# Optimization experiments

Hardware: AMD Instinct MI355X
Metric: run time of the kernel (lower is better)

## Reference

```python
import jax, jax.numpy as jnp
import numpy as np

B, N, C, R, E = 8, 4096, 128, 16, 65536


def setup_inputs() -> dict:
    key = jax.random.key(0)
    ks = jax.random.split(key, 8)
    node_features = jax.random.normal(ks[0], (B, N, C), dtype=jnp.float32)
    edge_index = jax.random.randint(ks[1], (B, 2, E), 0, N, dtype=jnp.int64)
    edge_type = jax.random.randint(ks[2], (B, E), 0, R, dtype=jnp.int64)
    s = 1.0 / np.sqrt(C)
    rel_weight = jax.random.uniform(ks[3], (R, C, C), jnp.float32, -s, s)
    root_weight = jax.random.uniform(ks[4], (C, C), jnp.float32, -s, s)
    rgcn_bias = jnp.zeros((C,), jnp.float32)
    lin_weight = jax.random.uniform(ks[5], (C, 1), jnp.float32, -s, s)
    lin_bias = jnp.zeros((1,), jnp.float32)
    return {
        'node_features': node_features,
        'edge_index': edge_index,
        'edge_type': edge_type,
        'rel_weight': rel_weight,
        'root_weight': root_weight,
        'rgcn_bias': rgcn_bias,
        'lin_weight': lin_weight,
        'lin_bias': lin_bias,
    }


def _rgcn_score(node_features, edge_index, edge_type, rel_weight, root_weight,
                rgcn_bias, lin_weight, lin_bias):
    # Flatten batch of graphs into one big disjoint graph (as batch_rgcn does).
    x = node_features.reshape(B * N, C)
    offs = (jnp.arange(B, dtype=edge_index.dtype) * N)[:, None, None]  # (B,1,1)
    ei = (edge_index + offs).transpose(1, 0, 2).reshape(2, B * E)  # (2, B*E)
    et = edge_type.reshape(B * E)
    src, dst = ei[0], ei[1]

    x_src = x[src]  # (B*E, C) gathered source features
    # root transform + bias (RGCNConv root_weight + bias)
    out = x @ root_weight + rgcn_bias  # (B*N, C)
    # per-relation mean aggregation; mean(W_r x_j) == W_r mean(x_j)
    for r in range(R):
        mask = (et == r).astype(x.dtype)  # (B*E,)
        s = jax.ops.segment_sum(x_src * mask[:, None], dst, num_segments=B * N)
        cnt = jax.ops.segment_sum(mask, dst, num_segments=B * N)
        mean = jnp.where(cnt[:, None] > 0, s / jnp.maximum(cnt, 1.0)[:, None], 0.0)
        out = out + mean @ rel_weight[r]

    out = jax.nn.relu(out)  # dropout is identity at eval
    scores = (out @ lin_weight + lin_bias).reshape(B, N)
    return scores


def reference(node_features, edge_index, edge_type, rel_weight, root_weight,
              rgcn_bias, lin_weight, lin_bias):
    return _rgcn_score(node_features, edge_index, edge_type, rel_weight,
                       root_weight, rgcn_bias, lin_weight, lin_bias)
```

## Files before the change

### kernel.cpp

```cpp
#include <hip/hip_runtime.h>

#define BB 8
#define NN 4096
#define CC 128
#define RR 16
#define EE 65536
#define NNODES 32768
#define NEDGES 524288
#define BCAP  48
#define SCE   15
#define NT    32
#define ALP   136

typedef unsigned short ushort_t;
typedef short bf16x8 __attribute__((ext_vector_type(8)));
typedef float f32x4 __attribute__((ext_vector_type(4)));

__device__ __forceinline__ unsigned short f2b(float f) {
    unsigned u = __builtin_bit_cast(unsigned, f);
    unsigned r = (u + 0x7fffu + ((u >> 16) & 1u)) >> 16;
    return (unsigned short)r;
}
__device__ __forceinline__ float b2f(unsigned short s) {
    return __builtin_bit_cast(float, (unsigned)s << 16);
}
__device__ __forceinline__ float ldf(const void* p, int j, int isbf) {
    return isbf ? b2f(((const ushort_t*)p)[j]) : ((const float*)p)[j];
}
__device__ __forceinline__ int ldi(const int* p, int j, int is64) {
    return p[j << is64];
}
__device__ __forceinline__ unsigned cvtpk(float lo, float hi) {
    unsigned r;
    asm("v_cvt_pk_bf16_f32 %0, %1, %2" : "=v"(r) : "v"(lo), "v"(hi));
    return r;
}

#define GSUM8(u, sb) do { \
    s[sb+0] += __builtin_bit_cast(float, (u).x << 16); \
    s[sb+1] += __builtin_bit_cast(float, (u).x & 0xffff0000u); \
    s[sb+2] += __builtin_bit_cast(float, (u).y << 16); \
    s[sb+3] += __builtin_bit_cast(float, (u).y & 0xffff0000u); \
    s[sb+4] += __builtin_bit_cast(float, (u).z << 16); \
    s[sb+5] += __builtin_bit_cast(float, (u).z & 0xffff0000u); \
    s[sb+6] += __builtin_bit_cast(float, (u).w << 16); \
    s[sb+7] += __builtin_bit_cast(float, (u).w & 0xffff0000u); \
} while (0)

__global__ __launch_bounds__(256) void prep_k(const void* __restrict__ x,
                                              const void* __restrict__ relw,
                                              const void* __restrict__ rootw,
                                              const int* __restrict__ ei,
                                              const int* __restrict__ et,
                                              ushort_t* __restrict__ Xb,
                                              ushort_t* __restrict__ WT3,
                                              int* __restrict__ dcnt,
                                              int* __restrict__ bucket,
                                              int isbf, int w64i, int w64t) {
    int bx = blockIdx.x, t = threadIdx.x;
    if (bx < 512) {
        int b = bx & 7;
        #pragma unroll
        for (int i = 0; i < 4; ++i) {
            int e = (bx >> 3) * 1024 + i * 256 + t;
            int src = ldi(ei, (b * 2) * EE + e, w64i);
            int dst = ldi(ei, (b * 2 + 1) * EE + e, w64i);
            int r = ldi(et, (b << 16) + e, w64t);
            int gd = (b << 12) + dst;
            int pos = atomicAdd(&dcnt[gd << 4], 1);
            if (pos < BCAP)
                bucket[gd * BCAP + pos] = (((b << 12) + src) << 4) | r;
        }
    } else if (bx < 1024) {
        int bx2 = bx - 512;
        int base = (bx2 & 7) * 65536 + (bx2 >> 3) * 256 + t;
        #pragma unroll
        for (int i = 0; i < 4; ++i) {
            int tid = base + i * 16384;
            if (isbf) {
                ((uint4*)Xb)[tid] = ((const uint4*)x)[tid];
            } else {
                const float4* xf = (const float4*)x;
                float4 a = xf[2 * tid], b = xf[2 * tid + 1];
                ushort4 o0, o1;
                o0.x = f2b(a.x); o0.y = f2b(a.y); o0.z = f2b(a.z); o0.w = f2b(a.w);
                o1.x = f2b(b.x); o1.y = f2b(b.y); o1.z = f2b(b.z); o1.w = f2b(b.w);
                ((ushort4*)Xb)[2 * tid] = o0; ((ushort4*)Xb)[2 * tid + 1] = o1;
            }
        }
    } else {
        __shared__ ushort_t Ls[128 * 40];
        int mb = bx - 1024;
        int mat = mb >> 2, chunk = mb & 3;
        const void* src = (mat == 16) ? rootw : relw;
        int soff = (mat == 16) ? 0 : mat * 16384;
        int k0 = chunk * 32;
        #pragma unroll
        for (int i = 0; i < 16; ++i) {
            int idx = t + i * 256;
            int k = idx >> 7, c = idx & 127;
            Ls[c * 40 + k] = f2b(ldf(src, soff + (k0 + k) * 128 + c, isbf));
        }
        __syncthreads();
        #pragma unroll
        for (int i = 0; i < 2; ++i) {
            int idx = t + i * 256;
            int cg = idx >> 6, lane = idx & 63;
            int lrow = lane & 15, lq = lane >> 4;
            uint4 v = *(const uint4*)(&Ls[(cg * 16 + lrow) * 40 + lq * 8]);
            *(uint4*)(WT3 + ((size_t)((mat * 4 + chunk) * 8 + cg)) * 512 + lane * 8) = v;
        }
    }
}

__global__ __launch_bounds__(512, 4) void agg_k(const ushort_t* __restrict__ Xb,
                                                const ushort_t* __restrict__ WT3,
                                                const int* __restrict__ dcnt,
                                                const int* __restrict__ bucket,
                                                const void* __restrict__ bias,
                                                const void* __restrict__ linw,
                                                const void* __restrict__ linb,
                                                void* __restrict__ out,
                                                int isbf) {
    __shared__ int scnt[NT * 16];
    __shared__ ushort_t srt[NT * 16 * 16];
    __shared__ ushort_t A[2][NT * ALP];
    __shared__ float red[NT][5];
    int bx = blockIdx.x, t = threadIdx.x;
    int n0 = (bx & 7) * NN + (bx >> 3) * NT;

    scnt[t & 511] = 0;
    __syncthreads();

    {
        int ns16 = t >> 4, ts16 = t & 15;
        int gn16 = n0 + ns16;
        int nc = dcnt[gn16 << 4]; if (nc > BCAP) nc = BCAP;
        const int* bk = bucket + gn16 * BCAP;
        for (int j = ts16; j < nc; j += 16) {
            int v = bk[j];
            int row = (ns16 << 4) + (v & 15);
            int pos = atomicAdd(&scnt[row], 1);
            if (pos < SCE)
                srt[(row << 4) + 1 + pos] = (ushort_t)((unsigned)v >> 4);
        }
    }
    __syncthreads();
    srt[t << 4] = (ushort_t)scnt[t];
    __syncthreads();

    int wave = t >> 6, lane = t & 63, lrow = lane & 15, lq = lane >> 4;
    int tg = t & 255;
    int nsub = tg >> 3, tsub = tg & 7;
    int gn = n0 + nsub;
    int offA = tsub * 8, offB = 64 + tsub * 8;
    f32x4 acc[2][2] = {};

    if (wave >= 4) {
        int row = nsub << 4;
        uint4 q0 = *(const uint4*)(&srt[row << 4]);
        int cf = q0.x & 0xffffu; int ce = cf > SCE ? SCE : cf;
        float s[16];
        #pragma unroll
        for (int j = 0; j < 16; ++j) s[j] = 0.f;
        for (int e = 0; e < ce; ++e) {
            int gs = srt[(row << 4) + 1 + e];
            const ushort_t* xr = Xb + (size_t)gs * 128;
            uint4 ua = *(const uint4*)(xr + offA), ub = *(const uint4*)(xr + offB);
            GSUM8(ua, 0); GSUM8(ub, 8);
        }
        float w = (cf > 0) ? 1.0f / (float)cf : 0.f;
        uint4 va, vb;
        va.x = cvtpk(s[0] * w, s[1] * w);   va.y = cvtpk(s[2] * w, s[3] * w);
        va.z = cvtpk(s[4] * w, s[5] * w);   va.w = cvtpk(s[6] * w, s[7] * w);
        vb.x = cvtpk(s[8] * w, s[9] * w);   vb.y = cvtpk(s[10] * w, s[11] * w);
        vb.z = cvtpk(s[12] * w, s[13] * w); vb.w = cvtpk(s[14] * w, s[15] * w);
        *(uint4*)(&A[0][nsub * ALP + offA]) = va;
        *(uint4*)(&A[0][nsub * ALP + offB]) = vb;
    }
    __syncthreads();

    for (int p = 0; p < 17; ++p) {
        int np = p + 1;
        if (wave < 4) {
            const ushort_t* Ap = A[p & 1];
            const ushort_t* bw = WT3 + (size_t)p * 16384 + (wave * 2) * 512 + lane * 8;
            __builtin_amdgcn_s_setprio(1);
            #pragma unroll
            for (int ks = 0; ks < 4; ++ks) {
                int k0 = ks * 32 + lq * 8;
                bf16x8 a0 = *(const bf16x8*)(&Ap[lrow * ALP + k0]);
                bf16x8 a1 = *(const bf16x8*)(&Ap[(16 + lrow) * ALP + k0]);
                bf16x8 b0 = *(const bf16x8*)(bw + ks * 4096);
                bf16x8 b1 = *(const bf16x8*)(bw + ks * 4096 + 512);
                acc[0][0] = __builtin_amdgcn_mfma_f32_16x16x32_bf16(a0, b0, acc[0][0], 0, 0, 0);
                acc[0][1] = __builtin_amdgcn_mfma_f32_16x16x32_bf16(a0, b1, acc[0][1], 0, 0, 0);
                acc[1][0] = __builtin_amdgcn_mfma_f32_16x16x32_bf16(a1, b0, acc[1][0], 0, 0, 0);
                acc[1][1] = __builtin_amdgcn_mfma_f32_16x16x32_bf16(a1, b1, acc[1][1], 0, 0, 0);
            }
            __builtin_amdgcn_s_setprio(0);
        } else if (np < 16) {
            int row = (nsub << 4) + np;
            uint4 q0 = *(const uint4*)(&srt[row << 4]);
            int cf = q0.x & 0xffffu; int ce = cf > SCE ? SCE : cf;
            int e0 = q0.x >> 16, e1 = q0.y & 0xffffu, e2 = q0.y >> 16, e3 = q0.z & 0xffffu;
            uint4 r0a, r0b, r1a, r1b, r2a, r2b, r3a, r3b;
            if (ce > 0) { const ushort_t* xr = Xb + (size_t)e0 * 128; r0a = *(const uint4*)(xr + offA); r0b = *(const uint4*)(xr + offB); }
            if (ce > 1) { const ushort_t* xr = Xb + (size_t)e1 * 128; r1a = *(const uint4*)(xr + offA); r1b = *(const uint4*)(xr + offB); }
            if (ce > 2) { const ushort_t* xr = Xb + (size_t)e2 * 128; r2a = *(const uint4*)(xr + offA); r2b = *(const uint4*)(xr + offB); }
            if (ce > 3) { const ushort_t* xr = Xb + (size_t)e3 * 128; r3a = *(const uint4*)(xr + offA); r3b = *(const uint4*)(xr + offB); }
            float s[16];
            #pragma unroll
            for (int j = 0; j < 16; ++j) s[j] = 0.f;
            if (ce > 0) { GSUM8(r0a, 0); GSUM8(r0b, 8); }
            if (ce > 1) { GSUM8(r1a, 0); GSUM8(r1b, 8); }
            if (ce > 2) { GSUM8(r2a, 0); GSUM8(r2b, 8); }
            if (ce > 3) { GSUM8(r3a, 0); GSUM8(r3b, 8); }
            if (ce > 4) {
                for (int e4 = 4; e4 < ce; ++e4) {
                    int gs = srt[(row << 4) + 1 + e4];
                    const ushort_t* xr = Xb + (size_t)gs * 128;
                    uint4 ta = *(const uint4*)(xr + offA), tb = *(const uint4*)(xr + offB);
                    GSUM8(ta, 0); GSUM8(tb, 8);
                }
            }
            float w = (cf > 0) ? 1.0f / (float)cf : 0.f;
            uint4 va, vb;
            va.x = cvtpk(s[0] * w, s[1] * w);   va.y = cvtpk(s[2] * w, s[3] * w);
            va.z = cvtpk(s[4] * w, s[5] * w);   va.w = cvtpk(s[6] * w, s[7] * w);
            vb.x = cvtpk(s[8] * w, s[9] * w);   vb.y = cvtpk(s[10] * w, s[11] * w);
            vb.z = cvtpk(s[12] * w, s[13] * w); vb.w = cvtpk(s[14] * w, s[15] * w);
            *(uint4*)(&A[np & 1][nsub * ALP + offA]) = va;
            *(uint4*)(&A[np & 1][nsub * ALP + offB]) = vb;
        } else if (np == 16) {
            const ushort_t* xr = Xb + (size_t)gn * 128;
            uint4 r0a = *(const uint4*)(xr + offA), r0b = *(const uint4*)(xr + offB);
            *(uint4*)(&A[np & 1][nsub * ALP + offA]) = r0a;
            *(uint4*)(&A[np & 1][nsub * ALP + offB]) = r0b;
        }
        if (p < 16) __syncthreads();
    }

    if (wave < 4) {
        int wn = wave << 5;
        int c0 = wn + lrow, c1 = wn + 16 + lrow;
        float bi0 = ldf(bias, c0, isbf), bi1 = ldf(bias, c1, isbf);
        float lw0 = ldf(linw, c0, isbf), lw1 = ldf(linw, c1, isbf);
        #pragma unroll
        for (int mi = 0; mi < 2; ++mi)
            #pragma unroll
            for (int rg = 0; rg < 4; ++rg) {
                float p = fmaxf(acc[mi][0][rg] + bi0, 0.f) * lw0
                        + fmaxf(acc[mi][1][rg] + bi1, 0.f) * lw1;
                p += __shfl_xor(p, 1, 64);
                p += __shfl_xor(p, 2, 64);
                p += __shfl_xor(p, 4, 64);
                p += __shfl_xor(p, 8, 64);
                if (lrow == 0) red[mi * 16 + lq * 4 + rg][wave] = p;
            }
    }
    __syncthreads();
    if (t < NT) {
        float res = red[t][0] + red[t][1] + red[t][2] + red[t][3] + ldf(linb, 0, isbf);
        if (isbf) ((ushort_t*)out)[n0 + t] = f2b(res);
        else      ((float*)out)[n0 + t] = res;
    }
}

extern "C" void kernel_launch(void* const* d_in, const int* in_sizes, int n_in,
                              void* d_out, int out_size, void* d_ws, size_t ws_size,
                              hipStream_t stream) {
    const void* x     = d_in[0];
    const int*  ei    = (const int*)d_in[1];
    const int*  et    = (const int*)d_in[2];
    const void* relw  = d_in[3];
    const void* rootw = d_in[4];
    const void* bias  = d_in[5];
    const void* linw  = d_in[6];
    const void* linb  = d_in[7];

    int isbf = (in_sizes[0] == BB * NN * CC * 2);
    int w64i = (in_sizes[1] == BB * 2 * EE * 8);
    int w64t = (in_sizes[2] == BB * EE * 8);

    const size_t WS_NEED = 17334272;
    if (ws_size < WS_NEED) return;

    char* ws = (char*)d_ws;
    ushort_t* Xb     = (ushort_t*)(ws);
    ushort_t* WT3    = (ushort_t*)(ws + 8388608);
    int*      dcnt   = (int*)(ws + 8945664);
    int*      bucket = (int*)(ws + 11042816);

    hipMemsetAsync(dcnt, 0, 2097152, stream);
    prep_k<<<1092, 256, 0, stream>>>(x, relw, rootw, ei, et, Xb, WT3, dcnt, bucket,
                                     isbf, w64i, w64t);
    agg_k<<<1024, 512, 0, stream>>>(Xb, WT3, dcnt, bucket, bias, linw, linb, d_out, isbf);
}
```

Baseline: 153.6 us.

## Merge producer and MFMA waves into one 256-thread software-pipelined loop

The aggregation kernel previously used 512 threads, with four waves doing MFMA and four waves gathering neighbour features into a double-buffered LDS tile. Now 256 threads do both jobs. Each wave issues the global gathers for stage p+2 into registers, runs the MFMAs for stage p, then finishes the reduction for stage p+1 into the other LDS buffer. The aim is to hide gather latency behind MFMA work inside each wave and to drop the idle half of the block. The cost is higher register pressure from the two in-flight prefetch sets, and fewer waves per block to hide latency.

```diff
diff --git a/kernel.cpp b/kernel.cpp
--- a/kernel.cpp
+++ b/kernel.cpp
@@ -113,7 +113,72 @@
     }
 }
 
-__global__ __launch_bounds__(512, 4) void agg_k(const ushort_t* __restrict__ Xb,
+#define STAGE(k, a0_,b0_,a1_,b1_,a2_,b2_,a3_,b3_, cf_,ce_,row_) do { \
+    if ((k) < 16) { \
+        row_ = (nsub << 4) + (k); \
+        uint4 q0 = *(const uint4*)(&srt[row_ << 4]); \
+        cf_ = q0.x & 0xffffu; ce_ = cf_ > SCE ? SCE : cf_; \
+        int e0 = q0.x >> 16, e1 = q0.y & 0xffffu, e2 = q0.y >> 16, e3 = q0.z & 0xffffu; \
+        if (ce_ > 0) { const ushort_t* xr = Xb + (size_t)e0 * 128; a0_ = *(const uint4*)(xr + offA); b0_ = *(const uint4*)(xr + offB); } \
+        if (ce_ > 1) { const ushort_t* xr = Xb + (size_t)e1 * 128; a1_ = *(const uint4*)(xr + offA); b1_ = *(const uint4*)(xr + offB); } \
+        if (ce_ > 2) { const ushort_t* xr = Xb + (size_t)e2 * 128; a2_ = *(const uint4*)(xr + offA); b2_ = *(const uint4*)(xr + offB); } \
+        if (ce_ > 3) { const ushort_t* xr = Xb + (size_t)e3 * 128; a3_ = *(const uint4*)(xr + offA); b3_ = *(const uint4*)(xr + offB); } \
+    } else if ((k) == 16) { \
+        const ushort_t* xr = Xb + (size_t)gn * 128; \
+        a0_ = *(const uint4*)(xr + offA); b0_ = *(const uint4*)(xr + offB); \
+        cf_ = -1; ce_ = 0; row_ = 0; \
+    } \
+} while (0)
+
+#define FINISH(AB, a0_,b0_,a1_,b1_,a2_,b2_,a3_,b3_, cf_,ce_,row_) do { \
+    if (cf_ < 0) {                           \
+        *(uint4*)(&A[AB][nsub * ALP + offA]) = a0_; \
+        *(uint4*)(&A[AB][nsub * ALP + offB]) = b0_; \
+    } else { \
+        float s[16]; \
+        _Pragma("unroll") for (int j = 0; j < 16; ++j) s[j] = 0.f; \
+        if (ce_ > 0) { GSUM8(a0_, 0); GSUM8(b0_, 8); } \
+        if (ce_ > 1) { GSUM8(a1_, 0); GSUM8(b1_, 8); } \
+        if (ce_ > 2) { GSUM8(a2_, 0); GSUM8(b2_, 8); } \
+        if (ce_ > 3) { GSUM8(a3_, 0); GSUM8(b3_, 8); } \
+        if (ce_ > 4) {                       \
+            for (int e4 = 4; e4 < ce_; ++e4) { \
+                int gs = srt[(row_ << 4) + 1 + e4]; \
+                const ushort_t* xr = Xb + (size_t)gs * 128; \
+                uint4 ta = *(const uint4*)(xr + offA), tb = *(const uint4*)(xr + offB); \
+                GSUM8(ta, 0); GSUM8(tb, 8); \
+            } \
+        } \
+        float w = (cf_ > 0) ? 1.0f / (float)cf_ : 0.f; \
+        uint4 va, vb; \
+        va.x = cvtpk(s[0] * w, s[1] * w);   va.y = cvtpk(s[2] * w, s[3] * w); \
+        va.z = cvtpk(s[4] * w, s[5] * w);   va.w = cvtpk(s[6] * w, s[7] * w); \
+        vb.x = cvtpk(s[8] * w, s[9] * w);   vb.y = cvtpk(s[10] * w, s[11] * w); \
+        vb.z = cvtpk(s[12] * w, s[13] * w); vb.w = cvtpk(s[14] * w, s[15] * w); \
+        *(uint4*)(&A[AB][nsub * ALP + offA]) = va; \
+        *(uint4*)(&A[AB][nsub * ALP + offB]) = vb; \
+    } \
+} while (0)
+
+#define MFMACL(AB, p) do { \
+    const ushort_t* bw = WT3 + (size_t)(p) * 16384 + (wave * 2) * 512 + lane * 8; \
+    __builtin_amdgcn_s_setprio(1); \
+    _Pragma("unroll") \
+    for (int ks = 0; ks < 4; ++ks) { \
+        int k0 = ks * 32 + lq * 8; \
+        bf16x8 a0 = *(const bf16x8*)(&A[AB][lrow * ALP + k0]); \
+        bf16x8 a1 = *(const bf16x8*)(&A[AB][(16 + lrow) * ALP + k0]); \
+        bf16x8 b0 = *(const bf16x8*)(bw + ks * 4096); \
+        bf16x8 b1 = *(const bf16x8*)(bw + ks * 4096 + 512); \
+        acc[0][0] = __builtin_amdgcn_mfma_f32_16x16x32_bf16(a0, b0, acc[0][0], 0, 0, 0); \
+        acc[0][1] = __builtin_amdgcn_mfma_f32_16x16x32_bf16(a0, b1, acc[0][1], 0, 0, 0); \
+        acc[1][0] = __builtin_amdgcn_mfma_f32_16x16x32_bf16(a1, b0, acc[1][0], 0, 0, 0); \
+        acc[1][1] = __builtin_amdgcn_mfma_f32_16x16x32_bf16(a1, b1, acc[1][1], 0, 0, 0); \
+    } \
+    __builtin_amdgcn_s_setprio(0); \
+} while (0)
+
+__global__ __launch_bounds__(256, 4) void agg_k(const ushort_t* __restrict__ Xb,
                                                 const ushort_t* __restrict__ WT3,
                                                 const int* __restrict__ dcnt,
                                                 const int* __restrict__ bucket,
@@ -129,34 +194,33 @@
     int bx = blockIdx.x, t = threadIdx.x;
     int n0 = (bx & 7) * NN + (bx >> 3) * NT;
 
-    scnt[t & 511] = 0;
-    __syncthreads();
-
-    {
-        int ns16 = t >> 4, ts16 = t & 15;
-        int gn16 = n0 + ns16;
-        int nc = dcnt[gn16 << 4]; if (nc > BCAP) nc = BCAP;
-        const int* bk = bucket + gn16 * BCAP;
-        for (int j = ts16; j < nc; j += 16) {
-            int v = bk[j];
-            int row = (ns16 << 4) + (v & 15);
-            int pos = atomicAdd(&scnt[row], 1);
-            if (pos < SCE)
-                srt[(row << 4) + 1 + pos] = (ushort_t)((unsigned)v >> 4);
-        }
-    }
-    __syncthreads();
-    srt[t << 4] = (ushort_t)scnt[t];
-    __syncthreads();
-
-    int wave = t >> 6, lane = t & 63, lrow = lane & 15, lq = lane >> 4;
-    int tg = t & 255;
-    int nsub = tg >> 3, tsub = tg & 7;
+    scnt[t] = 0; scnt[256 + t] = 0;
+    __syncthreads();
+
+    int nsub = t >> 3, tsub = t & 7;
     int gn = n0 + nsub;
     int offA = tsub * 8, offB = 64 + tsub * 8;
+    int nc = dcnt[gn << 4]; if (nc > BCAP) nc = BCAP;
+    const int* bk = bucket + gn * BCAP;
+    for (int j = tsub; j < nc; j += 8) {
+        int v = bk[j];
+        int row = (nsub << 4) + (v & 15);
+        int pos = atomicAdd(&scnt[row], 1);
+        if (pos < SCE)
+            srt[(row << 4) + 1 + pos] = (ushort_t)((unsigned)v >> 4);
+    }
+    __syncthreads();
+    srt[t << 4] = (ushort_t)scnt[t];
+    srt[(t + 256) << 4] = (ushort_t)scnt[t + 256];
+    __syncthreads();
+
+    int wave = t >> 6, lane = t & 63, lrow = lane & 15, lq = lane >> 4;
     f32x4 acc[2][2] = {};
 
-    if (wave >= 4) {
+    uint4 p0a0, p0b0, p0a1, p0b1, p0a2, p0b2, p0a3, p0b3; int cf0, ce0, row0;
+    uint4 p1a0, p1b0, p1a1, p1b1, p1a2, p1b2, p1a3, p1b3; int cf1, ce1, row1;
+
+    {
         int row = nsub << 4;
         uint4 q0 = *(const uint4*)(&srt[row << 4]);
         int cf = q0.x & 0xffffu; int ce = cf > SCE ? SCE : cf;
@@ -178,87 +242,38 @@
         *(uint4*)(&A[0][nsub * ALP + offA]) = va;
         *(uint4*)(&A[0][nsub * ALP + offB]) = vb;
     }
-    __syncthreads();
-
-    for (int p = 0; p < 17; ++p) {
-        int np = p + 1;
-        if (wave < 4) {
-            const ushort_t* Ap = A[p & 1];
-            const ushort_t* bw = WT3 + (size_t)p * 16384 + (wave * 2) * 512 + lane * 8;
-            __builtin_amdgcn_s_setprio(1);
-            #pragma unroll
-            for (int ks = 0; ks < 4; ++ks) {
-                int k0 = ks * 32 + lq * 8;
-                bf16x8 a0 = *(const bf16x8*)(&Ap[lrow * ALP + k0]);
-                bf16x8 a1 = *(const bf16x8*)(&Ap[(16 + lrow) * ALP + k0]);
-                bf16x8 b0 = *(const bf16x8*)(bw + ks * 4096);
-                bf16x8 b1 = *(const bf16x8*)(bw + ks * 4096 + 512);
-                acc[0][0] = __builtin_amdgcn_mfma_f32_16x16x32_bf16(a0, b0, acc[0][0], 0, 0, 0);
-                acc[0][1] = __builtin_amdgcn_mfma_f32_16x16x32_bf16(a0, b1, acc[0][1], 0, 0, 0);
-                acc[1][0] = __builtin_amdgcn_mfma_f32_16x16x32_bf16(a1, b0, acc[1][0], 0, 0, 0);
-                acc[1][1] = __builtin_amdgcn_mfma_f32_16x16x32_bf16(a1, b1, acc[1][1], 0, 0, 0);
-            }
-            __builtin_amdgcn_s_setprio(0);
-        } else if (np < 16) {
-            int row = (nsub << 4) + np;
-            uint4 q0 = *(const uint4*)(&srt[row << 4]);
-            int cf = q0.x & 0xffffu; int ce = cf > SCE ? SCE : cf;
-            int e0 = q0.x >> 16, e1 = q0.y & 0xffffu, e2 = q0.y >> 16, e3 = q0.z & 0xffffu;
-            uint4 r0a, r0b, r1a, r1b, r2a, r2b, r3a, r3b;
-            if (ce > 0) { const ushort_t* xr = Xb + (size_t)e0 * 128; r0a = *(const uint4*)(xr + offA); r0b = *(const uint4*)(xr + offB); }
-            if (ce > 1) { const ushort_t* xr = Xb + (size_t)e1 * 128; r1a = *(const uint4*)(xr + offA); r1b = *(const uint4*)(xr + offB); }
-            if (ce > 2) { const ushort_t* xr = Xb + (size_t)e2 * 128; r2a = *(const uint4*)(xr + offA); r2b = *(const uint4*)(xr + offB); }
-            if (ce > 3) { const ushort_t* xr = Xb + (size_t)e3 * 128; r3a = *(const uint4*)(xr + offA); r3b = *(const uint4*)(xr + offB); }
-            float s[16];
-            #pragma unroll
-            for (int j = 0; j < 16; ++j) s[j] = 0.f;
-            if (ce > 0) { GSUM8(r0a, 0); GSUM8(r0b, 8); }
-            if (ce > 1) { GSUM8(r1a, 0); GSUM8(r1b, 8); }
-            if (ce > 2) { GSUM8(r2a, 0); GSUM8(r2b, 8); }
-            if (ce > 3) { GSUM8(r3a, 0); GSUM8(r3b, 8); }
-            if (ce > 4) {
-                for (int e4 = 4; e4 < ce; ++e4) {
-                    int gs = srt[(row << 4) + 1 + e4];
-                    const ushort_t* xr = Xb + (size_t)gs * 128;
-                    uint4 ta = *(const uint4*)(xr + offA), tb = *(const uint4*)(xr + offB);
-                    GSUM8(ta, 0); GSUM8(tb, 8);
-                }
-            }
-            float w = (cf > 0) ? 1.0f / (float)cf : 0.f;
-            uint4 va, vb;
-            va.x = cvtpk(s[0] * w, s[1] * w);   va.y = cvtpk(s[2] * w, s[3] * w);
-            va.z = cvtpk(s[4] * w, s[5] * w);   va.w = cvtpk(s[6] * w, s[7] * w);
-            vb.x = cvtpk(s[8] * w, s[9] * w);   vb.y = cvtpk(s[10] * w, s[11] * w);
-            vb.z = cvtpk(s[12] * w, s[13] * w); vb.w = cvtpk(s[14] * w, s[15] * w);
-            *(uint4*)(&A[np & 1][nsub * ALP + offA]) = va;
-            *(uint4*)(&A[np & 1][nsub * ALP + offB]) = vb;
-        } else if (np == 16) {
-            const ushort_t* xr = Xb + (size_t)gn * 128;
-            uint4 r0a = *(const uint4*)(xr + offA), r0b = *(const uint4*)(xr + offB);
-            *(uint4*)(&A[np & 1][nsub * ALP + offA]) = r0a;
-            *(uint4*)(&A[np & 1][nsub * ALP + offB]) = r0b;
-        }
-        if (p < 16) __syncthreads();
-    }
-
-    if (wave < 4) {
-        int wn = wave << 5;
-        int c0 = wn + lrow, c1 = wn + 16 + lrow;
-        float bi0 = ldf(bias, c0, isbf), bi1 = ldf(bias, c1, isbf);
-        float lw0 = ldf(linw, c0, isbf), lw1 = ldf(linw, c1, isbf);
-        #pragma unroll
-        for (int mi = 0; mi < 2; ++mi)
-            #pragma unroll
-            for (int rg = 0; rg < 4; ++rg) {
-                float p = fmaxf(acc[mi][0][rg] + bi0, 0.f) * lw0
-                        + fmaxf(acc[mi][1][rg] + bi1, 0.f) * lw1;
-                p += __shfl_xor(p, 1, 64);
-                p += __shfl_xor(p, 2, 64);
-                p += __shfl_xor(p, 4, 64);
-                p += __shfl_xor(p, 8, 64);
-                if (lrow == 0) red[mi * 16 + lq * 4 + rg][wave] = p;
-            }
-    }
+    STAGE(1, p0a0,p0b0,p0a1,p0b1,p0a2,p0b2,p0a3,p0b3, cf0,ce0,row0);
+    __syncthreads();
+
+    for (int pb = 0; pb < 8; ++pb) {
+        int p0 = 2 * pb, p1 = p0 + 1;
+        STAGE(p0 + 2, p1a0,p1b0,p1a1,p1b1,p1a2,p1b2,p1a3,p1b3, cf1,ce1,row1);
+        MFMACL(0, p0);
+        FINISH(1, p0a0,p0b0,p0a1,p0b1,p0a2,p0b2,p0a3,p0b3, cf0,ce0,row0);
+        __syncthreads();
+        STAGE(p1 + 2, p0a0,p0b0,p0a1,p0b1,p0a2,p0b2,p0a3,p0b3, cf0,ce0,row0);
+        MFMACL(1, p1);
+        FINISH(0, p1a0,p1b0,p1a1,p1b1,p1a2,p1b2,p1a3,p1b3, cf1,ce1,row1);
+        __syncthreads();
+    }
+    MFMACL(0, 16);
+
+    int wn = wave << 5;
+    int c0 = wn + lrow, c1 = wn + 16 + lrow;
+    float bi0 = ldf(bias, c0, isbf), bi1 = ldf(bias, c1, isbf);
+    float lw0 = ldf(linw, c0, isbf), lw1 = ldf(linw, c1, isbf);
+    #pragma unroll
+    for (int mi = 0; mi < 2; ++mi)
+        #pragma unroll
+        for (int rg = 0; rg < 4; ++rg) {
+            float p = fmaxf(acc[mi][0][rg] + bi0, 0.f) * lw0
+                    + fmaxf(acc[mi][1][rg] + bi1, 0.f) * lw1;
+            p += __shfl_xor(p, 1, 64);
+            p += __shfl_xor(p, 2, 64);
+            p += __shfl_xor(p, 4, 64);
+            p += __shfl_xor(p, 8, 64);
+            if (lrow == 0) red[mi * 16 + lq * 4 + rg][wave] = p;
+        }
     __syncthreads();
     if (t < NT) {
         float res = red[t][0] + red[t][1] + red[t][2] + red[t][3] + ldf(linb, 0, isbf);
@@ -295,5 +310,5 @@
     hipMemsetAsync(dcnt, 0, 2097152, stream);
     prep_k<<<1092, 256, 0, stream>>>(x, relw, rootw, ei, et, Xb, WT3, dcnt, bucket,
                                      isbf, w64i, w64t);
-    agg_k<<<1024, 512, 0, stream>>>(Xb, WT3, dcnt, bucket, bias, linw, linb, d_out, isbf);
-}
+    agg_k<<<1024, 256, 0, stream>>>(Xb, WT3, dcnt, bucket, bias, linw, linb, d_out, isbf);
+}
```

Result: slower. 161.6 us (+5.2%).
